# Kernel optimization log

Hardware: AMD Instinct MI355X
Metric: run time of the kernel (lower is better)

The kernel has to match this reference:

```python
import jax, jax.numpy as jnp
import numpy as np

B, N, D, H = 4, 2048, 512, 8
HD = D // H
NUM_BUCKETS, MAX_EXACT, MAX_DIST = 44, 28, 2048
_BAND_RANGES = [range(38, 44), range(34, 40), range(28, 35), range(20, 28),
                range(13, 21), range(7, 14), range(3, 9), range(0, 6)]


def _band_mask():
    m = np.zeros((NUM_BUCKETS, H), dtype=np.float32)
    for h, band in enumerate(_BAND_RANGES):
        for j in band:
            m[j, h] = 1.0
    return jnp.asarray(m)


def _rel_bucket(n):
    # T5-style causal relative-position buckets: exact for d<MAX_EXACT, log-spaced above.
    i = jnp.arange(n)[:, None]
    j = jnp.arange(n)[None, :]
    d = jnp.maximum(i - j, 0)
    safe = jnp.maximum(d, 1).astype(jnp.float32)
    logb = MAX_EXACT + (jnp.log(safe / MAX_EXACT)
                        / np.log(MAX_DIST / MAX_EXACT)
                        * (NUM_BUCKETS - MAX_EXACT)).astype(jnp.int32)
    return jnp.where(d < MAX_EXACT, d, jnp.minimum(logb, NUM_BUCKETS - 1))  # [n,n]


def setup_inputs() -> dict:
    key = jax.random.key(0)
    ks = jax.random.split(key, 12)
    s = 0.02
    return {
        "x": jax.random.normal(ks[0], (B, N, D), jnp.float32),
        "k_delta": jax.random.normal(ks[1], (B, H, N, HD), jnp.float32) * 0.1,
        "v_delta": jax.random.normal(ks[2], (B, H, N, HD), jnp.float32) * 0.1,
        "qkv_w": jax.random.normal(ks[3], (D, 3 * D), jnp.float32) * s,
        "qkv_b": jnp.zeros((3 * D,), jnp.float32),
        "gate_w": jax.random.normal(ks[4], (D, D), jnp.float32) * s,
        "gate_b": jnp.zeros((D,), jnp.float32),
        "out_w": jax.random.normal(ks[5], (D, D), jnp.float32) * s,
        "out_b": jnp.zeros((D,), jnp.float32),
        "pos_bias": jax.random.normal(ks[6], (NUM_BUCKETS, H), jnp.float32) * 0.1,
        "if_gain": jnp.ones((H,), jnp.float32),
    }


def reference(x, k_delta, v_delta, qkv_w, qkv_b, gate_w, gate_b,
              out_w, out_b, pos_bias, if_gain):
    b, n, d = x.shape
    band = _band_mask()
    # hard per-head banding of the relative bias
    eff_bias = pos_bias * band + (1.0 - band) * (-100.0)           # [44,H]
    qkv = x @ qkv_w + qkv_b                                         # [B,N,3D]
    q, k, v = jnp.split(qkv, 3, axis=-1)
    q = q.reshape(b, n, H, HD).transpose(0, 2, 1, 3)                # [B,H,N,HD]
    k = k.reshape(b, n, H, HD).transpose(0, 2, 1, 3) + k_delta
    v = v.reshape(b, n, H, HD).transpose(0, 2, 1, 3) + v_delta
    bucket = _rel_bucket(n)                                         # [N,N] int
    bias = eff_bias[bucket].transpose(2, 0, 1)                      # [H,N,N]
    scores = jnp.einsum("bhid,bhjd->bhij", q, k) / np.sqrt(HD) + bias[None]
    causal = jnp.tril(jnp.ones((n, n), bool))
    scores = jnp.where(causal[None, None], scores, -1e9)
    attn = jax.nn.softmax(scores, axis=-1)
    out = jnp.einsum("bhij,bhjd->bhid", attn, v)                    # [B,H,N,HD]
    out = out * if_gain[None, :, None, None]                        # IF gain
    out_flat = out.transpose(0, 2, 1, 3).reshape(b, n, d)
    gate = jax.nn.sigmoid(x @ gate_w + gate_b)                      # output gating
    return (out_flat * gate) @ out_w + out_b
```

## Files before the change

kernel.cpp:

```cpp
#include <hip/hip_runtime.h>
#include <cmath>

typedef unsigned short u16;
typedef unsigned short u16x4 __attribute__((ext_vector_type(4)));
typedef unsigned short u16x8 __attribute__((ext_vector_type(8)));
typedef __bf16 bf16x8 __attribute__((ext_vector_type(8)));
typedef float f32x4 __attribute__((ext_vector_type(4)));

#define HNUM 8
#define HDIM 64
#define BATCH 4
#define NSEQ 2048
#define DMODEL 512
#define NFUSED 2048
#define LP 72
#define CP 132
#define NSLOT 14

__device__ __forceinline__ u16 f2bf(float f) {
  unsigned int u = __builtin_bit_cast(unsigned int, f);
  u += 0x7fffu + ((u >> 16) & 1u);
  return (u16)(u >> 16);
}

__device__ __forceinline__ float bf2f(u16 v) {
  unsigned int u = ((unsigned int)v) << 16;
  return __builtin_bit_cast(float, u);
}

__device__ __forceinline__ f32x4 mfma_bf16(u16x8 a, u16x8 b, f32x4 c) {
  return __builtin_amdgcn_mfma_f32_16x16x32_bf16(
      __builtin_bit_cast(bf16x8, a), __builtin_bit_cast(bf16x8, b), c, 0, 0, 0);
}

__device__ __forceinline__ void gload16(u16* lds, const u16* g) {
  __builtin_amdgcn_global_load_lds(
      (const __attribute__((address_space(1))) void*)g,
      (__attribute__((address_space(3))) void*)lds, 16, 0, 0);
}

template <int ROWS>
__device__ __forceinline__ void stage_tile(u16* lds, const u16* g, int tid) {
  #pragma unroll
  for (int i = 0; i < ROWS / 64; ++i) {
    const int t = i * 256 + tid;
    const int row = t >> 2;
    const int ch = (t & 3) ^ ((row >> 1) & 3);
    gload16(lds + t * 8, g + (size_t)row * DMODEL + ch * 8);
  }
}
__device__ __forceinline__ int swz_off(int row, int lg) {
  return row * 32 + ((lg ^ ((row >> 1) & 3)) << 3);
}

__global__ __launch_bounds__(256) void cvt_bf16_kernel(
    const float* __restrict__ in, u16* __restrict__ out, int n8) {
  int i = blockIdx.x * 256 + threadIdx.x;
  if (i >= n8) return;
  const float4 f0 = *(const float4*)(in + i * 8);
  const float4 f1 = *(const float4*)(in + i * 8 + 4);
  u16x8 pk;
  pk[0] = f2bf(f0.x); pk[1] = f2bf(f0.y); pk[2] = f2bf(f0.z); pk[3] = f2bf(f0.w);
  pk[4] = f2bf(f1.x); pk[5] = f2bf(f1.y); pk[6] = f2bf(f1.z); pk[7] = f2bf(f1.w);
  *(u16x8*)(out + i * 8) = pk;
}

__global__ __launch_bounds__(256) void transpose_w_kernel(
    const float* __restrict__ W, u16* __restrict__ Wt, int K, int N) {
  __shared__ float tile[32][33];
  const int n0 = blockIdx.x * 32, k0 = blockIdx.y * 32;
  const int tx = threadIdx.x & 31, ty = threadIdx.x >> 5;
  #pragma unroll
  for (int yy = ty; yy < 32; yy += 8)
    tile[yy][tx] = W[(size_t)(k0 + yy) * N + n0 + tx];
  __syncthreads();
  #pragma unroll
  for (int yy = ty; yy < 32; yy += 8)
    Wt[(size_t)(n0 + yy) * K + k0 + tx] = f2bf(tile[tx][yy]);
}

__global__ __launch_bounds__(256) void transpose_v_kernel(
    const u16* __restrict__ v, u16* __restrict__ vT) {
  __shared__ u16 t[64][LP];
  const int n0 = blockIdx.x * 64;
  const size_t bh = blockIdx.y;
  const int r = threadIdx.x >> 2, c0 = (threadIdx.x & 3) << 4;
  const u16* src = v + (bh * NSEQ + n0 + r) * HDIM + c0;
  u16x8 a0 = *(const u16x8*)src;
  u16x8 a1 = *(const u16x8*)(src + 8);
  #pragma unroll
  for (int j = 0; j < 8; ++j) {
    t[c0 + j][r] = a0[j];
    t[c0 + 8 + j][r] = a1[j];
  }
  __syncthreads();
  u16x8 o0 = *(const u16x8*)&t[r][c0];
  u16x8 o1 = *(const u16x8*)&t[r][c0 + 8];
  u16* dst = vT + (bh * HDIM + r) * NSEQ + n0 + c0;
  *(u16x8*)dst = o0;
  *(u16x8*)(dst + 8) = o1;
}

__global__ __launch_bounds__(256) void bias_tab_kernel(
    const float* __restrict__ pos_bias, float* __restrict__ tab) {
  int d = blockIdx.x * 256 + threadIdx.x;
  if (d >= NSEQ) return;
  int bkt;
  if (d < 28) {
    bkt = d;
  } else {
    double t = log((double)d / 28.0) / log(2048.0 / 28.0) * 16.0;
    int ti = 28 + (int)t;
    bkt = ti < 43 ? ti : 43;
  }
  const int lo[8] = {38, 34, 28, 20, 13, 7, 3, 0};
  const int hi[8] = {44, 40, 35, 28, 21, 14, 9, 6};
  #pragma unroll
  for (int h = 0; h < HNUM; ++h) {
    bool inb = (bkt >= lo[h]) && (bkt < hi[h]);
    tab[h * NSEQ + d] = inb ? pos_bias[bkt * HNUM + h] : -100.0f;
  }
}

__global__ __launch_bounds__(256) void gemm_fused(
    const u16* __restrict__ Abf, const u16* __restrict__ Wt,
    const float* __restrict__ qkv_b, const float* __restrict__ gate_b,
    const float* __restrict__ kdelta, const float* __restrict__ vdelta,
    u16* __restrict__ qbf, u16* __restrict__ kbf, u16* __restrict__ vbf,
    u16* __restrict__ gate) {
  __shared__ __align__(16) u16 S[6][128 * 32];

  const int bid = blockIdx.y * 16 + blockIdx.x;
  const int nb = (bid & 7) * 128 + (bid >> 3);
  const int m0 = (nb >> 4) * 128;
  const int n0 = (nb & 15) * 128;

  const int tid = threadIdx.x;
  const int w = tid >> 6, l = tid & 63, li = l & 15, lg = l >> 4;
  const int wr = w >> 1, wc = w & 1;

  f32x4 acc[4][4];
  #pragma unroll
  for (int i = 0; i < 4; ++i)
    #pragma unroll
    for (int j = 0; j < 4; ++j) acc[i][j] = f32x4{0.f, 0.f, 0.f, 0.f};

  const u16* Ab = Abf + (size_t)m0 * DMODEL;
  const u16* Bb = Wt + (size_t)n0 * DMODEL;

  stage_tile<128>(S[0], Ab, tid);
  stage_tile<128>(S[3], Bb, tid);
  stage_tile<128>(S[1], Ab + 32, tid);
  stage_tile<128>(S[4], Bb + 32, tid);

  #pragma unroll
  for (int kt = 0; kt < 16; ++kt) {
    if (kt + 2 < 16) {
      stage_tile<128>(S[(kt + 2) % 3], Ab + (kt + 2) * 32, tid);
      stage_tile<128>(S[3 + (kt + 2) % 3], Bb + (kt + 2) * 32, tid);
    }
    if (kt < 14)       asm volatile("s_waitcnt vmcnt(8)" ::: "memory");
    else if (kt == 14) asm volatile("s_waitcnt vmcnt(4)" ::: "memory");
    else               asm volatile("s_waitcnt vmcnt(0)" ::: "memory");
    __builtin_amdgcn_s_barrier();
    __builtin_amdgcn_sched_barrier(0);
    const u16* Asb = S[kt % 3];
    const u16* Bsb = S[3 + kt % 3];
    u16x8 af[4], bfr[4];
    #pragma unroll
    for (int mt = 0; mt < 4; ++mt)
      af[mt] = *(const u16x8*)&Asb[swz_off(wr * 64 + mt * 16 + li, lg)];
    #pragma unroll
    for (int nt = 0; nt < 4; ++nt)
      bfr[nt] = *(const u16x8*)&Bsb[swz_off(wc * 64 + nt * 16 + li, lg)];
    asm volatile("s_waitcnt lgkmcnt(0)" ::: "memory");
    __builtin_amdgcn_sched_barrier(0);
    #pragma unroll
    for (int mt = 0; mt < 4; ++mt)
      #pragma unroll
      for (int nt = 0; nt < 4; ++nt)
        acc[mt][nt] = mfma_bf16(af[mt], bfr[nt], acc[mt][nt]);
    __builtin_amdgcn_s_barrier();
    __builtin_amdgcn_sched_barrier(0);
  }

  u16* Ct = S[0];
  const int seg = n0 >> 9;
  #pragma unroll
  for (int nt = 0; nt < 4; ++nt) {
    const int col = wc * 64 + nt * 16 + li;
    const int colg = n0 + col;
    const float bv = (seg < 3) ? qkv_b[colg] : gate_b[colg & 511];
    #pragma unroll
    for (int mt = 0; mt < 4; ++mt) {
      const int row = wr * 64 + mt * 16 + lg * 4;
      #pragma unroll
      for (int r = 0; r < 4; ++r)
        Ct[(row + r) * CP + col] = f2bf(acc[mt][nt][r] + bv);
    }
  }
  __syncthreads();

  const int nin = n0 & 511;
  #pragma unroll
  for (int p = 0; p < 8; ++p) {
    const int row = p * 16 + (tid >> 4);
    const int cc = (tid & 15) * 8;
    const int rg = m0 + row;
    const int b = rg >> 11, n = rg & 2047;
    u16x8 cv = *(const u16x8*)&Ct[row * CP + cc];
    if (seg == 3) {
      u16x8 o;
      #pragma unroll
      for (int j = 0; j < 8; ++j)
        o[j] = f2bf(1.f / (1.f + __expf(-bf2f(cv[j]))));
      *(u16x8*)&gate[(size_t)rg * DMODEL + nin + cc] = o;
    } else {
      const int hh = (nin + cc) >> 6, hd = (nin + cc) & 63;
      const size_t hidx = (((size_t)b * HNUM + hh) * NSEQ + n) * HDIM + hd;
      if (seg == 0) {
        u16x8 o;
        #pragma unroll
        for (int j = 0; j < 8; ++j) o[j] = f2bf(bf2f(cv[j]) * 0.125f);
        *(u16x8*)&qbf[hidx] = o;
      } else {
        const float* dp = (seg == 1 ? kdelta : vdelta) + hidx;
        float4 d0 = *(const float4*)dp;
        float4 d1 = *(const float4*)(dp + 4);
        u16x8 o;
        o[0] = f2bf(bf2f(cv[0]) + d0.x); o[1] = f2bf(bf2f(cv[1]) + d0.y);
        o[2] = f2bf(bf2f(cv[2]) + d0.z); o[3] = f2bf(bf2f(cv[3]) + d0.w);
        o[4] = f2bf(bf2f(cv[4]) + d1.x); o[5] = f2bf(bf2f(cv[5]) + d1.y);
        o[6] = f2bf(bf2f(cv[6]) + d1.z); o[7] = f2bf(bf2f(cv[7]) + d1.w);
        *(u16x8*)&((seg == 1) ? kbf : vbf)[hidx] = o;
      }
    }
  }
}

__global__ __launch_bounds__(256) void gemm_out(
    const u16* __restrict__ Abf, const u16* __restrict__ Wt,
    const float* __restrict__ bias, float* __restrict__ outf) {
  __shared__ __align__(16) u16 As[3][64 * 32];
  __shared__ __align__(16) u16 Bs[3][128 * 32];

  const int m0 = blockIdx.y * 64, n0 = blockIdx.x * 128;
  const int tid = threadIdx.x;
  const int w = tid >> 6, l = tid & 63, li = l & 15, lg = l >> 4;
  const int wr = w >> 1, wc = w & 1;

  f32x4 acc[2][4];
  #pragma unroll
  for (int i = 0; i < 2; ++i)
    #pragma unroll
    for (int j = 0; j < 4; ++j) acc[i][j] = f32x4{0.f, 0.f, 0.f, 0.f};

  const u16* Ab = Abf + (size_t)m0 * DMODEL;
  const u16* Bb = Wt + (size_t)n0 * DMODEL;

  stage_tile<64>(As[0], Ab, tid);
  stage_tile<128>(Bs[0], Bb, tid);
  stage_tile<64>(As[1], Ab + 32, tid);
  stage_tile<128>(Bs[1], Bb + 32, tid);

  #pragma unroll
  for (int kt = 0; kt < 16; ++kt) {
    if (kt + 2 < 16) {
      stage_tile<64>(As[(kt + 2) % 3], Ab + (kt + 2) * 32, tid);
      stage_tile<128>(Bs[(kt + 2) % 3], Bb + (kt + 2) * 32, tid);
    }
    if (kt < 14)       asm volatile("s_waitcnt vmcnt(6)" ::: "memory");
    else if (kt == 14) asm volatile("s_waitcnt vmcnt(3)" ::: "memory");
    else               asm volatile("s_waitcnt vmcnt(0)" ::: "memory");
    __builtin_amdgcn_s_barrier();
    __builtin_amdgcn_sched_barrier(0);
    const u16* Asb = As[kt % 3];
    const u16* Bsb = Bs[kt % 3];
    u16x8 af[2], bfr[4];
    #pragma unroll
    for (int mt = 0; mt < 2; ++mt)
      af[mt] = *(const u16x8*)&Asb[swz_off(wr * 32 + mt * 16 + li, lg)];
    #pragma unroll
    for (int nt = 0; nt < 4; ++nt)
      bfr[nt] = *(const u16x8*)&Bsb[swz_off(wc * 64 + nt * 16 + li, lg)];
    asm volatile("s_waitcnt lgkmcnt(0)" ::: "memory");
    __builtin_amdgcn_sched_barrier(0);
    #pragma unroll
    for (int mt = 0; mt < 2; ++mt)
      #pragma unroll
      for (int nt = 0; nt < 4; ++nt)
        acc[mt][nt] = mfma_bf16(af[mt], bfr[nt], acc[mt][nt]);
    __builtin_amdgcn_s_barrier();
    __builtin_amdgcn_sched_barrier(0);
  }

  #pragma unroll
  for (int nt = 0; nt < 4; ++nt) {
    const int colg = n0 + wc * 64 + nt * 16 + li;
    const float bv = bias[colg];
    #pragma unroll
    for (int mt = 0; mt < 2; ++mt) {
      #pragma unroll
      for (int r = 0; r < 4; ++r) {
        const int rowg = m0 + wr * 32 + mt * 16 + lg * 4 + r;
        outf[(size_t)rowg * DMODEL + colg] = acc[mt][nt][r] + bv;
      }
    }
  }
}

__global__ __launch_bounds__(256) void attn_kernel(
    const u16* __restrict__ qbf, const u16* __restrict__ kbf,
    const u16* __restrict__ vbfT, const float* __restrict__ bias_tab,
    const float* __restrict__ if_gain, const u16* __restrict__ gate,
    u16* __restrict__ attn_out, u16* __restrict__ partO,
    float* __restrict__ partM, float* __restrict__ partL) {
  __shared__ __align__(16) u16 Ks[64][LP];
  __shared__ __align__(16) u16 Vt[64][LP];
  __shared__ __align__(16) u16 Pl[4][16][LP];

  static const int DMINW[8] = {408, 139, 26, 18, 11, 5, 1, 0};
  static const int DMAXW[8] = {2049, 702, 185, 29, 22, 15, 10, 7};
  static const int DMINS[8] = {412, 143, 30, 22, 15, 9, 5, 2};
  static const int SH[19] = {0,0,0,0,0,0,0,0, 1,1,1,1, 2,2, 3,4,5,6,7};
  static const int SC[19] = {0,1,2,3,4,5,6,7, 0,1,2,3, 0,1, 0,0,0,0,0};
  static const int SN[19] = {8,8,8,8,8,8,8,8, 4,4,4,4, 2,2, 1,1,1,1,1};

  const int slot = blockIdx.x >> 7;
  const int rem = blockIdx.x & 127;
  const int qt = 31 - (rem >> 2);
  const int b = rem & 3;
  const int h = SH[slot], ch = SC[slot], nc = SN[slot];
  const int bh = b * HNUM + h;
  const int q0 = qt * 64;
  const int tid = threadIdx.x;
  const int w = tid >> 6, l = tid & 63, li = l & 15, lg = l >> 4;

  const u16* qrow = qbf + ((size_t)bh * NSEQ + q0 + w * 16 + li) * HDIM;
  u16x8 qf0 = *(const u16x8*)(qrow + lg * 8);
  u16x8 qf1 = *(const u16x8*)(qrow + 32 + lg * 8);

  const bool pure = q0 >= DMINS[h];
  int kv_lo = 0, kv_hi = q0 + 64;
  if (pure) {
    int lo = q0 - DMAXW[h];
    kv_lo = (lo > 0 ? lo : 0) & ~63;
    kv_hi = q0 + 64 - DMINW[h];
  }
  const int t0 = kv_lo >> 6, t1 = (kv_hi - 1) >> 6;
  const int len = t1 - t0 + 1;
  const int ta = t0 + (len * ch) / nc;
  const int tb = t0 + (len * (ch + 1)) / nc - 1;

  const int srow = tid >> 2;
  const int scb = (tid & 3) << 4;
  const float* btab = bias_tab + h * NSEQ;

  float mrun = -INFINITY, lrun = 0.f;
  f32x4 O[4] = {{0.f,0.f,0.f,0.f},{0.f,0.f,0.f,0.f},
                {0.f,0.f,0.f,0.f},{0.f,0.f,0.f,0.f}};

  for (int tt = ta; tt <= tb; ++tt) {
    const int kv0 = tt << 6;
    {
      const size_t kbase = ((size_t)bh * NSEQ + kv0 + srow) * HDIM + scb;
      u16x8 k0 = *(const u16x8*)(kbf + kbase);
      u16x8 k1 = *(const u16x8*)(kbf + kbase + 8);
      const size_t vbase = ((size_t)bh * HDIM + srow) * NSEQ + kv0 + scb;
      u16x8 v0 = *(const u16x8*)(vbfT + vbase);
      u16x8 v1 = *(const u16x8*)(vbfT + vbase + 8);
      *(u16x8*)&Ks[srow][scb] = k0;
      *(u16x8*)&Ks[srow][scb + 8] = k1;
      *(u16x8*)&Vt[srow][scb] = v0;
      *(u16x8*)&Vt[srow][scb + 8] = v1;
    }
    __syncthreads();

    f32x4 s[4];
    #pragma unroll
    for (int t = 0; t < 4; ++t) {
      u16x8 a0 = *(const u16x8*)&Ks[t * 16 + li][lg * 8];
      u16x8 a1 = *(const u16x8*)&Ks[t * 16 + li][32 + lg * 8];
      f32x4 acc = {0.f, 0.f, 0.f, 0.f};
      acc = mfma_bf16(a0, qf0, acc);
      acc = mfma_bf16(a1, qf1, acc);
      s[t] = acc;
    }

    const int D0 = (q0 + w * 16 + li) - kv0 - lg * 4;
    float rm = -1e30f;
    #pragma unroll
    for (int t = 0; t < 4; ++t) {
      #pragma unroll
      for (int r = 0; r < 4; ++r) {
        int d = D0 - 16 * t - r;
        float sv = s[t][r];
        sv = (d >= 0) ? (sv + btab[d]) : -1e30f;
        s[t][r] = sv;
        rm = fmaxf(rm, sv);
      }
    }
    rm = fmaxf(rm, __shfl_xor(rm, 16, 64));
    rm = fmaxf(rm, __shfl_xor(rm, 32, 64));
    const float mn = fmaxf(mrun, rm);
    const float f = __expf(mrun - mn);
    mrun = mn;
    float ps = 0.f;
    #pragma unroll
    for (int t = 0; t < 4; ++t) {
      #pragma unroll
      for (int r = 0; r < 4; ++r) {
        float p = __expf(s[t][r] - mn);
        s[t][r] = p;
        ps += p;
      }
    }
    ps += __shfl_xor(ps, 16, 64);
    ps += __shfl_xor(ps, 32, 64);
    lrun = lrun * f + ps;

    #pragma unroll
    for (int t = 0; t < 4; ++t) {
      u16x4 pk;
      pk[0] = f2bf(s[t][0]); pk[1] = f2bf(s[t][1]);
      pk[2] = f2bf(s[t][2]); pk[3] = f2bf(s[t][3]);
      *(u16x4*)&Pl[w][li][t * 16 + lg * 4] = pk;
    }

    float fr[4];
    #pragma unroll
    for (int r = 0; r < 4; ++r) fr[r] = __shfl(f, lg * 4 + r, 64);
    #pragma unroll
    for (int dt = 0; dt < 4; ++dt) {
      O[dt][0] *= fr[0]; O[dt][1] *= fr[1];
      O[dt][2] *= fr[2]; O[dt][3] *= fr[3];
    }
    __syncthreads();

    #pragma unroll
    for (int ks = 0; ks < 2; ++ks) {
      u16x8 pA = *(const u16x8*)&Pl[w][li][ks * 32 + lg * 8];
      #pragma unroll
      for (int dt = 0; dt < 4; ++dt) {
        u16x8 vB = *(const u16x8*)&Vt[dt * 16 + li][ks * 32 + lg * 8];
        O[dt] = mfma_bf16(pA, vB, O[dt]);
      }
    }
    __syncthreads();
  }

  if (nc == 1) {
    const float gain = if_gain[h];
    float linv[4];
    #pragma unroll
    for (int r = 0; r < 4; ++r)
      linv[r] = gain / __shfl(lrun, lg * 4 + r, 64);
    #pragma unroll
    for (int r = 0; r < 4; ++r) {
      const int i = q0 + w * 16 + lg * 4 + r;
      const size_t base = ((size_t)b * NSEQ + i) * DMODEL + h * HDIM + li;
      #pragma unroll
      for (int dt = 0; dt < 4; ++dt) {
        const float g = bf2f(gate[base + dt * 16]);
        attn_out[base + dt * 16] = f2bf(O[dt][r] * linv[r] * g);
      }
    }
  } else {
    const int sbase = (b * 32 + qt) * NSLOT + slot;
    #pragma unroll
    for (int r = 0; r < 4; ++r) {
      const int rl = w * 16 + lg * 4 + r;
      #pragma unroll
      for (int dt = 0; dt < 4; ++dt)
        partO[(size_t)sbase * 4096 + rl * 64 + dt * 16 + li] = f2bf(O[dt][r]);
    }
    if (lg == 0) {
      partM[sbase * 64 + w * 16 + li] = mrun;
      partL[sbase * 64 + w * 16 + li] = lrun;
    }
  }
}

__global__ __launch_bounds__(256) void combine_kernel(
    const u16* __restrict__ partO, const float* __restrict__ partM,
    const float* __restrict__ partL, const float* __restrict__ if_gain,
    const u16* __restrict__ gate, u16* __restrict__ attn_out) {
  const int b = blockIdx.x & 3, qt = blockIdx.x >> 2;
  const int tid = threadIdx.x;
  const int row = tid >> 2, d0 = (tid & 3) << 4;
  static const int HNC[3] = {8, 4, 2};
  static const int HS0[3] = {0, 8, 12};

  #pragma unroll
  for (int hc = 0; hc < 3; ++hc) {
    const int nc = HNC[hc], s0 = HS0[hc];
    const int sbase = (b * 32 + qt) * NSLOT + s0;
    float m[8];
    float M = -INFINITY;
    #pragma unroll
    for (int c = 0; c < 8; ++c) {
      m[c] = (c < nc) ? partM[(sbase + c) * 64 + row] : -INFINITY;
      M = fmaxf(M, m[c]);
    }
    float wch[8];
    float den = 0.f;
    #pragma unroll
    for (int c = 0; c < 8; ++c) {
      wch[c] = (c < nc) ? __expf(m[c] - M) : 0.f;
      if (c < nc) den += wch[c] * partL[(sbase + c) * 64 + row];
    }
    float num[16];
    #pragma unroll
    for (int j = 0; j < 16; ++j) num[j] = 0.f;
    #pragma unroll
    for (int c = 0; c < 8; ++c) {
      if (c < nc) {
        const u16* op = partO + (size_t)(sbase + c) * 4096 + row * 64 + d0;
        u16x8 o0 = *(const u16x8*)op;
        u16x8 o1 = *(const u16x8*)(op + 8);
        #pragma unroll
        for (int j = 0; j < 8; ++j) {
          num[j]     += wch[c] * bf2f(o0[j]);
          num[8 + j] += wch[c] * bf2f(o1[j]);
        }
      }
    }
    const float inv = if_gain[hc] / den;
    const size_t obase =
        ((size_t)b * NSEQ + qt * 64 + row) * DMODEL + hc * HDIM + d0;
    u16x8 g0 = *(const u16x8*)(gate + obase);
    u16x8 g1 = *(const u16x8*)(gate + obase + 8);
    u16x8 r0, r1;
    #pragma unroll
    for (int j = 0; j < 8; ++j) {
      r0[j] = f2bf(num[j] * inv * bf2f(g0[j]));
      r1[j] = f2bf(num[8 + j] * inv * bf2f(g1[j]));
    }
    *(u16x8*)(attn_out + obase) = r0;
    *(u16x8*)(attn_out + obase + 8) = r1;
  }
}

extern "C" void kernel_launch(void* const* d_in, const int* in_sizes, int n_in,
                              void* d_out, int out_size, void* d_ws,
                              size_t ws_size, hipStream_t stream) {
  const float* x       = (const float*)d_in[0];
  const float* k_delta = (const float*)d_in[1];
  const float* v_delta = (const float*)d_in[2];
  const float* qkv_w   = (const float*)d_in[3];
  const float* qkv_b   = (const float*)d_in[4];
  const float* gate_w  = (const float*)d_in[5];
  const float* gate_b  = (const float*)d_in[6];
  const float* out_w   = (const float*)d_in[7];
  const float* out_b   = (const float*)d_in[8];
  const float* pos_bias = (const float*)d_in[9];
  const float* if_gain  = (const float*)d_in[10];
  float* out = (float*)d_out;
  char* ws = (char*)d_ws;

  u16*   xbf      = (u16*)(ws + 0);
  u16*   qbf      = (u16*)(ws + 8388608);
  u16*   kbf      = (u16*)(ws + 16777216);
  u16*   vbf      = (u16*)(ws + 25165824);
  u16*   vbfT     = (u16*)(ws + 33554432);
  u16*   gate_buf = (u16*)(ws + 41943040);
  u16*   fused_wt = (u16*)(ws + 50331648);
  u16*   out_wt   = (u16*)(ws + 52428800);
  float* bias_tab = (float*)(ws + 52953088);
  u16*   partO = (u16*)(ws + 53018624);
  float* partM = (float*)(ws + 67698688);
  float* partL = (float*)(ws + 68157440);
  u16*   attn_buf = vbf;

  cvt_bf16_kernel<<<dim3(2048), dim3(256), 0, stream>>>(
      x, xbf, BATCH * NSEQ * DMODEL / 8);
  transpose_w_kernel<<<dim3(48, 16), dim3(256), 0, stream>>>(
      qkv_w, fused_wt, DMODEL, 3 * DMODEL);
  transpose_w_kernel<<<dim3(16, 16), dim3(256), 0, stream>>>(
      gate_w, fused_wt + (size_t)3 * DMODEL * DMODEL, DMODEL, DMODEL);
  transpose_w_kernel<<<dim3(16, 16), dim3(256), 0, stream>>>(
      out_w, out_wt, DMODEL, DMODEL);
  bias_tab_kernel<<<dim3(8), dim3(256), 0, stream>>>(pos_bias, bias_tab);

  gemm_fused<<<dim3(16, 64), dim3(256), 0, stream>>>(
      xbf, fused_wt, qkv_b, gate_b, k_delta, v_delta,
      qbf, kbf, vbf, gate_buf);

  transpose_v_kernel<<<dim3(32, 32), dim3(256), 0, stream>>>(vbf, vbfT);

  attn_kernel<<<dim3(2432), dim3(256), 0, stream>>>(
      qbf, kbf, vbfT, bias_tab, if_gain, gate_buf, attn_buf,
      partO, partM, partL);

  combine_kernel<<<dim3(128), dim3(256), 0, stream>>>(
      partO, partM, partL, if_gain, gate_buf, attn_buf);

  gemm_out<<<dim3(4, 128), dim3(256), 0, stream>>>(
      attn_buf, out_wt, out_b, out);

  (void)in_sizes; (void)n_in; (void)out_size; (void)ws_size;
}
```

Measured before the change: 100.9 us.

## Enlarge fused QKV/gate GEMM tiles to 256x256 with 512 threads and BK=64

The fused projection GEMM moves from 128x128 tiles with 256 threads and a triple-buffered BK=32 pipeline to 256x256 tiles with 512 threads, double-buffered BK=64 stages and an 8-way XOR swizzle. The epilogue is written out in two 128-row halves through a padded LDS staging buffer. The larger tile raises arithmetic intensity and halves global reloads of A and B. In exchange it uses 128KB of LDS and 128 accumulator registers per thread, which limits occupancy, and it launches only 256 blocks, close to the CU count.

```diff
diff --git a/kernel.cpp b/kernel.cpp
--- a/kernel.cpp
+++ b/kernel.cpp
@@ -14,7 +14,7 @@
 #define DMODEL 512
 #define NFUSED 2048
 #define LP 72
-#define CP 132
+#define CPE 272
 #define NSLOT 14
 
 __device__ __forceinline__ u16 f2bf(float f) {
@@ -37,6 +37,18 @@
   __builtin_amdgcn_global_load_lds(
       (const __attribute__((address_space(1))) void*)g,
       (__attribute__((address_space(3))) void*)lds, 16, 0, 0);
+}
+
+__device__ __forceinline__ void stage256(u16* lds, const u16* g, int tid) {
+  #pragma unroll
+  for (int i = 0; i < 4; ++i) {
+    const int s = i * 512 + tid;
+    const int row = s >> 3, ch = s & 7;
+    gload16(lds + s * 8, g + (size_t)row * DMODEL + ((ch ^ (row & 7)) << 3));
+  }
+}
+__device__ __forceinline__ int swz64(int row, int c) {
+  return row * 64 + ((c ^ (row & 7)) << 3);
 }
 
 template <int ROWS>
@@ -122,119 +134,127 @@
   }
 }
 
-__global__ __launch_bounds__(256) void gemm_fused(
+__global__ __launch_bounds__(512) void gemm_fused(
     const u16* __restrict__ Abf, const u16* __restrict__ Wt,
     const float* __restrict__ qkv_b, const float* __restrict__ gate_b,
     const float* __restrict__ kdelta, const float* __restrict__ vdelta,
     u16* __restrict__ qbf, u16* __restrict__ kbf, u16* __restrict__ vbf,
     u16* __restrict__ gate) {
-  __shared__ __align__(16) u16 S[6][128 * 32];
-
-  const int bid = blockIdx.y * 16 + blockIdx.x;
-  const int nb = (bid & 7) * 128 + (bid >> 3);
-  const int m0 = (nb >> 4) * 128;
-  const int n0 = (nb & 15) * 128;
+  __shared__ __align__(16) u16 S[65536];
+  u16* SA[2] = {S, S + 16384};
+  u16* SB[2] = {S + 32768, S + 49152};
+
+  const int bid = blockIdx.x;
+  const int m0 = ((bid & 7) * 4 + ((bid >> 3) & 3)) * 256;
+  const int n0 = (bid >> 5) * 256;
 
   const int tid = threadIdx.x;
   const int w = tid >> 6, l = tid & 63, li = l & 15, lg = l >> 4;
-  const int wr = w >> 1, wc = w & 1;
-
-  f32x4 acc[4][4];
-  #pragma unroll
-  for (int i = 0; i < 4; ++i)
+  const int wm = w >> 2, wn = w & 3;
+
+  f32x4 acc[8][4];
+  #pragma unroll
+  for (int i = 0; i < 8; ++i)
     #pragma unroll
     for (int j = 0; j < 4; ++j) acc[i][j] = f32x4{0.f, 0.f, 0.f, 0.f};
 
   const u16* Ab = Abf + (size_t)m0 * DMODEL;
   const u16* Bb = Wt + (size_t)n0 * DMODEL;
 
-  stage_tile<128>(S[0], Ab, tid);
-  stage_tile<128>(S[3], Bb, tid);
-  stage_tile<128>(S[1], Ab + 32, tid);
-  stage_tile<128>(S[4], Bb + 32, tid);
-
-  #pragma unroll
-  for (int kt = 0; kt < 16; ++kt) {
-    if (kt + 2 < 16) {
-      stage_tile<128>(S[(kt + 2) % 3], Ab + (kt + 2) * 32, tid);
-      stage_tile<128>(S[3 + (kt + 2) % 3], Bb + (kt + 2) * 32, tid);
-    }
-    if (kt < 14)       asm volatile("s_waitcnt vmcnt(8)" ::: "memory");
-    else if (kt == 14) asm volatile("s_waitcnt vmcnt(4)" ::: "memory");
-    else               asm volatile("s_waitcnt vmcnt(0)" ::: "memory");
+  stage256(SA[0], Ab, tid);
+  stage256(SB[0], Bb, tid);
+
+  #pragma unroll
+  for (int kt = 0; kt < 8; ++kt) {
+    if (kt < 7) {
+      stage256(SA[(kt + 1) & 1], Ab + (kt + 1) * 64, tid);
+      stage256(SB[(kt + 1) & 1], Bb + (kt + 1) * 64, tid);
+      asm volatile("s_waitcnt vmcnt(8)" ::: "memory");
+    } else {
+      asm volatile("s_waitcnt vmcnt(0)" ::: "memory");
+    }
     __builtin_amdgcn_s_barrier();
     __builtin_amdgcn_sched_barrier(0);
-    const u16* Asb = S[kt % 3];
-    const u16* Bsb = S[3 + kt % 3];
-    u16x8 af[4], bfr[4];
-    #pragma unroll
-    for (int mt = 0; mt < 4; ++mt)
-      af[mt] = *(const u16x8*)&Asb[swz_off(wr * 64 + mt * 16 + li, lg)];
-    #pragma unroll
-    for (int nt = 0; nt < 4; ++nt)
-      bfr[nt] = *(const u16x8*)&Bsb[swz_off(wc * 64 + nt * 16 + li, lg)];
-    asm volatile("s_waitcnt lgkmcnt(0)" ::: "memory");
-    __builtin_amdgcn_sched_barrier(0);
-    #pragma unroll
-    for (int mt = 0; mt < 4; ++mt)
+    const u16* Asb = SA[kt & 1];
+    const u16* Bsb = SB[kt & 1];
+    #pragma unroll
+    for (int ks = 0; ks < 2; ++ks) {
+      u16x8 a[8], b[4];
+      #pragma unroll
+      for (int mt = 0; mt < 8; ++mt)
+        a[mt] = *(const u16x8*)&Asb[swz64(wm * 128 + mt * 16 + li, ks * 4 + lg)];
       #pragma unroll
       for (int nt = 0; nt < 4; ++nt)
-        acc[mt][nt] = mfma_bf16(af[mt], bfr[nt], acc[mt][nt]);
+        b[nt] = *(const u16x8*)&Bsb[swz64(wn * 64 + nt * 16 + li, ks * 4 + lg)];
+      asm volatile("s_waitcnt lgkmcnt(0)" ::: "memory");
+      __builtin_amdgcn_sched_barrier(0);
+      #pragma unroll
+      for (int mt = 0; mt < 8; ++mt)
+        #pragma unroll
+        for (int nt = 0; nt < 4; ++nt)
+          acc[mt][nt] = mfma_bf16(a[mt], b[nt], acc[mt][nt]);
+    }
     __builtin_amdgcn_s_barrier();
     __builtin_amdgcn_sched_barrier(0);
   }
 
-  u16* Ct = S[0];
+  u16* Ct = S;
   const int seg = n0 >> 9;
-  #pragma unroll
-  for (int nt = 0; nt < 4; ++nt) {
-    const int col = wc * 64 + nt * 16 + li;
-    const int colg = n0 + col;
-    const float bv = (seg < 3) ? qkv_b[colg] : gate_b[colg & 511];
-    #pragma unroll
-    for (int mt = 0; mt < 4; ++mt) {
-      const int row = wr * 64 + mt * 16 + lg * 4;
-      #pragma unroll
-      for (int r = 0; r < 4; ++r)
-        Ct[(row + r) * CP + col] = f2bf(acc[mt][nt][r] + bv);
-    }
-  }
-  __syncthreads();
-
   const int nin = n0 & 511;
   #pragma unroll
-  for (int p = 0; p < 8; ++p) {
-    const int row = p * 16 + (tid >> 4);
-    const int cc = (tid & 15) * 8;
-    const int rg = m0 + row;
-    const int b = rg >> 11, n = rg & 2047;
-    u16x8 cv = *(const u16x8*)&Ct[row * CP + cc];
-    if (seg == 3) {
-      u16x8 o;
-      #pragma unroll
-      for (int j = 0; j < 8; ++j)
-        o[j] = f2bf(1.f / (1.f + __expf(-bf2f(cv[j]))));
-      *(u16x8*)&gate[(size_t)rg * DMODEL + nin + cc] = o;
-    } else {
-      const int hh = (nin + cc) >> 6, hd = (nin + cc) & 63;
-      const size_t hidx = (((size_t)b * HNUM + hh) * NSEQ + n) * HDIM + hd;
-      if (seg == 0) {
+  for (int h = 0; h < 2; ++h) {
+    if (wm == h) {
+      #pragma unroll
+      for (int nt = 0; nt < 4; ++nt) {
+        const int col = wn * 64 + nt * 16 + li;
+        const int colg = n0 + col;
+        const float bv = (seg < 3) ? qkv_b[colg] : gate_b[colg & 511];
+        #pragma unroll
+        for (int mt = 0; mt < 8; ++mt) {
+          const int row = mt * 16 + lg * 4;
+          #pragma unroll
+          for (int r = 0; r < 4; ++r)
+            Ct[(row + r) * CPE + col] = f2bf(acc[mt][nt][r] + bv);
+        }
+      }
+    }
+    __syncthreads();
+    #pragma unroll
+    for (int p = 0; p < 8; ++p) {
+      const int idx = p * 512 + tid;
+      const int row = idx >> 5, ccol = (idx & 31) * 8;
+      const int rg = m0 + h * 128 + row;
+      const int bb = rg >> 11, n = rg & 2047;
+      u16x8 cv = *(const u16x8*)&Ct[row * CPE + ccol];
+      const int cws = nin + ccol;
+      if (seg == 3) {
         u16x8 o;
         #pragma unroll
-        for (int j = 0; j < 8; ++j) o[j] = f2bf(bf2f(cv[j]) * 0.125f);
-        *(u16x8*)&qbf[hidx] = o;
+        for (int j = 0; j < 8; ++j)
+          o[j] = f2bf(1.f / (1.f + __expf(-bf2f(cv[j]))));
+        *(u16x8*)&gate[(size_t)rg * DMODEL + cws] = o;
       } else {
-        const float* dp = (seg == 1 ? kdelta : vdelta) + hidx;
-        float4 d0 = *(const float4*)dp;
-        float4 d1 = *(const float4*)(dp + 4);
-        u16x8 o;
-        o[0] = f2bf(bf2f(cv[0]) + d0.x); o[1] = f2bf(bf2f(cv[1]) + d0.y);
-        o[2] = f2bf(bf2f(cv[2]) + d0.z); o[3] = f2bf(bf2f(cv[3]) + d0.w);
-        o[4] = f2bf(bf2f(cv[4]) + d1.x); o[5] = f2bf(bf2f(cv[5]) + d1.y);
-        o[6] = f2bf(bf2f(cv[6]) + d1.z); o[7] = f2bf(bf2f(cv[7]) + d1.w);
-        *(u16x8*)&((seg == 1) ? kbf : vbf)[hidx] = o;
-      }
-    }
+        const int hh = cws >> 6, hd = cws & 63;
+        const size_t hidx = (((size_t)bb * HNUM + hh) * NSEQ + n) * HDIM + hd;
+        if (seg == 0) {
+          u16x8 o;
+          #pragma unroll
+          for (int j = 0; j < 8; ++j) o[j] = f2bf(bf2f(cv[j]) * 0.125f);
+          *(u16x8*)&qbf[hidx] = o;
+        } else {
+          const float* dp = (seg == 1 ? kdelta : vdelta) + hidx;
+          float4 d0 = *(const float4*)dp;
+          float4 d1 = *(const float4*)(dp + 4);
+          u16x8 o;
+          o[0] = f2bf(bf2f(cv[0]) + d0.x); o[1] = f2bf(bf2f(cv[1]) + d0.y);
+          o[2] = f2bf(bf2f(cv[2]) + d0.z); o[3] = f2bf(bf2f(cv[3]) + d0.w);
+          o[4] = f2bf(bf2f(cv[4]) + d1.x); o[5] = f2bf(bf2f(cv[5]) + d1.y);
+          o[6] = f2bf(bf2f(cv[6]) + d1.z); o[7] = f2bf(bf2f(cv[7]) + d1.w);
+          *(u16x8*)&((seg == 1) ? kbf : vbf)[hidx] = o;
+        }
+      }
+    }
+    __syncthreads();
   }
 }
 
@@ -582,7 +602,7 @@
       out_w, out_wt, DMODEL, DMODEL);
   bias_tab_kernel<<<dim3(8), dim3(256), 0, stream>>>(pos_bias, bias_tab);
 
-  gemm_fused<<<dim3(16, 64), dim3(256), 0, stream>>>(
+  gemm_fused<<<dim3(256), dim3(512), 0, stream>>>(
       xbf, fused_wt, qkv_b, gate_b, k_delta, v_delta,
       qbf, kbf, vbf, gate_buf);
 
```

After: 98.54 us. 1.02x faster.

## Widen fused QKV/gate GEMM tile to 128x256 with 512 threads; merge weight transposes

Applied to the files above, without the earlier changes.

The fused projection GEMM moves from 128x128 tiles with 4 waves to 128x256 tiles with 8 waves in 512-thread blocks. This halves the grid and raises reuse of each staged A tile, and it uses a new XCD-aware block mapping and a staging helper. The three weight-transpose launches are merged into one kernel to cut launch overhead. The larger LDS footprint and 512-thread blocks may reduce occupancy.

```diff
diff --git a/kernel.cpp b/kernel.cpp
--- a/kernel.cpp
+++ b/kernel.cpp
@@ -12,9 +12,8 @@
 #define BATCH 4
 #define NSEQ 2048
 #define DMODEL 512
-#define NFUSED 2048
 #define LP 72
-#define CP 132
+#define CPE 264
 #define NSLOT 14
 
 __device__ __forceinline__ u16 f2bf(float f) {
@@ -37,6 +36,10 @@
   __builtin_amdgcn_global_load_lds(
       (const __attribute__((address_space(1))) void*)g,
       (__attribute__((address_space(3))) void*)lds, 16, 0, 0);
+}
+
+__device__ __forceinline__ int swz_off(int row, int lg) {
+  return row * 32 + ((lg ^ ((row >> 1) & 3)) << 3);
 }
 
 template <int ROWS>
@@ -49,8 +52,22 @@
     gload16(lds + t * 8, g + (size_t)row * DMODEL + ch * 8);
   }
 }
-__device__ __forceinline__ int swz_off(int row, int lg) {
-  return row * 32 + ((lg ^ ((row >> 1) & 3)) << 3);
+
+__device__ __forceinline__ void stageAB(u16* ldsA, u16* ldsB, const u16* gA,
+                                        const u16* gB, int tid) {
+  {
+    const int s = tid;
+    const int row = s >> 2;
+    const int ch = (s & 3) ^ ((row >> 1) & 3);
+    gload16(ldsA + s * 8, gA + (size_t)row * DMODEL + ch * 8);
+  }
+  #pragma unroll
+  for (int i = 0; i < 2; ++i) {
+    const int s = i * 512 + tid;
+    const int row = s >> 2;
+    const int ch = (s & 3) ^ ((row >> 1) & 3);
+    gload16(ldsB + s * 8, gB + (size_t)row * DMODEL + ch * 8);
+  }
 }
 
 __global__ __launch_bounds__(256) void cvt_bf16_kernel(
@@ -65,10 +82,19 @@
   *(u16x8*)(out + i * 8) = pk;
 }
 
-__global__ __launch_bounds__(256) void transpose_w_kernel(
-    const float* __restrict__ W, u16* __restrict__ Wt, int K, int N) {
+__global__ __launch_bounds__(256) void transpose_wall(
+    const float* __restrict__ qkv_w, const float* __restrict__ gate_w,
+    const float* __restrict__ out_w, u16* __restrict__ fused_wt,
+    u16* __restrict__ out_wt) {
   __shared__ float tile[32][33];
-  const int n0 = blockIdx.x * 32, k0 = blockIdx.y * 32;
+  const int bx = blockIdx.x;
+  const float* W;
+  u16* Wt;
+  int N, nb;
+  if (bx < 48)      { W = qkv_w;  Wt = fused_wt;                     N = 1536; nb = bx; }
+  else if (bx < 64) { W = gate_w; Wt = fused_wt + (size_t)1536 * 512; N = 512;  nb = bx - 48; }
+  else              { W = out_w;  Wt = out_wt;                       N = 512;  nb = bx - 64; }
+  const int n0 = nb * 32, k0 = blockIdx.y * 32;
   const int tx = threadIdx.x & 31, ty = threadIdx.x >> 5;
   #pragma unroll
   for (int yy = ty; yy < 32; yy += 8)
@@ -76,7 +102,7 @@
   __syncthreads();
   #pragma unroll
   for (int yy = ty; yy < 32; yy += 8)
-    Wt[(size_t)(n0 + yy) * K + k0 + tx] = f2bf(tile[tx][yy]);
+    Wt[(size_t)(n0 + yy) * DMODEL + k0 + tx] = f2bf(tile[tx][yy]);
 }
 
 __global__ __launch_bounds__(256) void transpose_v_kernel(
@@ -122,22 +148,24 @@
   }
 }
 
-__global__ __launch_bounds__(256) void gemm_fused(
+__global__ __launch_bounds__(512, 4) void gemm_fused(
     const u16* __restrict__ Abf, const u16* __restrict__ Wt,
     const float* __restrict__ qkv_b, const float* __restrict__ gate_b,
     const float* __restrict__ kdelta, const float* __restrict__ vdelta,
     u16* __restrict__ qbf, u16* __restrict__ kbf, u16* __restrict__ vbf,
     u16* __restrict__ gate) {
-  __shared__ __align__(16) u16 S[6][128 * 32];
-
-  const int bid = blockIdx.y * 16 + blockIdx.x;
-  const int nb = (bid & 7) * 128 + (bid >> 3);
-  const int m0 = (nb >> 4) * 128;
-  const int n0 = (nb & 15) * 128;
+  __shared__ __align__(16) u16 S[36864];
+  u16* SA3[3] = {S, S + 4096, S + 8192};
+  u16* SB3[3] = {S + 12288, S + 20480, S + 28672};
+
+  const int bid = blockIdx.x;
+  const int xcd = bid & 7, loc = bid >> 3;
+  const int m0 = (xcd * 8 + (loc & 7)) * 128;
+  const int n0 = (loc >> 3) * 256;
 
   const int tid = threadIdx.x;
   const int w = tid >> 6, l = tid & 63, li = l & 15, lg = l >> 4;
-  const int wr = w >> 1, wc = w & 1;
+  const int wm = w >> 2, wn = w & 3;
 
   f32x4 acc[4][4];
   #pragma unroll
@@ -148,31 +176,28 @@
   const u16* Ab = Abf + (size_t)m0 * DMODEL;
   const u16* Bb = Wt + (size_t)n0 * DMODEL;
 
-  stage_tile<128>(S[0], Ab, tid);
-  stage_tile<128>(S[3], Bb, tid);
-  stage_tile<128>(S[1], Ab + 32, tid);
-  stage_tile<128>(S[4], Bb + 32, tid);
+  stageAB(SA3[0], SB3[0], Ab, Bb, tid);
+  stageAB(SA3[1], SB3[1], Ab + 32, Bb + 32, tid);
 
   #pragma unroll
   for (int kt = 0; kt < 16; ++kt) {
-    if (kt + 2 < 16) {
-      stage_tile<128>(S[(kt + 2) % 3], Ab + (kt + 2) * 32, tid);
-      stage_tile<128>(S[3 + (kt + 2) % 3], Bb + (kt + 2) * 32, tid);
-    }
-    if (kt < 14)       asm volatile("s_waitcnt vmcnt(8)" ::: "memory");
-    else if (kt == 14) asm volatile("s_waitcnt vmcnt(4)" ::: "memory");
+    if (kt + 2 < 16)
+      stageAB(SA3[(kt + 2) % 3], SB3[(kt + 2) % 3],
+              Ab + (kt + 2) * 32, Bb + (kt + 2) * 32, tid);
+    if (kt < 14)       asm volatile("s_waitcnt vmcnt(6)" ::: "memory");
+    else if (kt == 14) asm volatile("s_waitcnt vmcnt(3)" ::: "memory");
     else               asm volatile("s_waitcnt vmcnt(0)" ::: "memory");
     __builtin_amdgcn_s_barrier();
     __builtin_amdgcn_sched_barrier(0);
-    const u16* Asb = S[kt % 3];
-    const u16* Bsb = S[3 + kt % 3];
+    const u16* Asb = SA3[kt % 3];
+    const u16* Bsb = SB3[kt % 3];
     u16x8 af[4], bfr[4];
     #pragma unroll
     for (int mt = 0; mt < 4; ++mt)
-      af[mt] = *(const u16x8*)&Asb[swz_off(wr * 64 + mt * 16 + li, lg)];
+      af[mt] = *(const u16x8*)&Asb[swz_off(wm * 64 + mt * 16 + li, lg)];
     #pragma unroll
     for (int nt = 0; nt < 4; ++nt)
-      bfr[nt] = *(const u16x8*)&Bsb[swz_off(wc * 64 + nt * 16 + li, lg)];
+      bfr[nt] = *(const u16x8*)&Bsb[swz_off(wn * 64 + nt * 16 + li, lg)];
     asm volatile("s_waitcnt lgkmcnt(0)" ::: "memory");
     __builtin_amdgcn_sched_barrier(0);
     #pragma unroll
@@ -184,40 +209,41 @@
     __builtin_amdgcn_sched_barrier(0);
   }
 
-  u16* Ct = S[0];
+  u16* Ct = S;
   const int seg = n0 >> 9;
+  const int nin = n0 & 511;
   #pragma unroll
   for (int nt = 0; nt < 4; ++nt) {
-    const int col = wc * 64 + nt * 16 + li;
+    const int col = wn * 64 + nt * 16 + li;
     const int colg = n0 + col;
     const float bv = (seg < 3) ? qkv_b[colg] : gate_b[colg & 511];
     #pragma unroll
     for (int mt = 0; mt < 4; ++mt) {
-      const int row = wr * 64 + mt * 16 + lg * 4;
+      const int row = wm * 64 + mt * 16 + lg * 4;
       #pragma unroll
       for (int r = 0; r < 4; ++r)
-        Ct[(row + r) * CP + col] = f2bf(acc[mt][nt][r] + bv);
+        Ct[(row + r) * CPE + col] = f2bf(acc[mt][nt][r] + bv);
     }
   }
   __syncthreads();
 
-  const int nin = n0 & 511;
   #pragma unroll
   for (int p = 0; p < 8; ++p) {
-    const int row = p * 16 + (tid >> 4);
-    const int cc = (tid & 15) * 8;
+    const int idx = p * 512 + tid;
+    const int row = idx >> 5, ccol = (idx & 31) * 8;
     const int rg = m0 + row;
-    const int b = rg >> 11, n = rg & 2047;
-    u16x8 cv = *(const u16x8*)&Ct[row * CP + cc];
+    const int bb = rg >> 11, n = rg & 2047;
+    u16x8 cv = *(const u16x8*)&Ct[row * CPE + ccol];
+    const int cws = nin + ccol;
     if (seg == 3) {
       u16x8 o;
       #pragma unroll
       for (int j = 0; j < 8; ++j)
         o[j] = f2bf(1.f / (1.f + __expf(-bf2f(cv[j]))));
-      *(u16x8*)&gate[(size_t)rg * DMODEL + nin + cc] = o;
+      *(u16x8*)&gate[(size_t)rg * DMODEL + cws] = o;
     } else {
-      const int hh = (nin + cc) >> 6, hd = (nin + cc) & 63;
-      const size_t hidx = (((size_t)b * HNUM + hh) * NSEQ + n) * HDIM + hd;
+      const int hh = cws >> 6, hd = cws & 63;
+      const size_t hidx = (((size_t)bb * HNUM + hh) * NSEQ + n) * HDIM + hd;
       if (seg == 0) {
         u16x8 o;
         #pragma unroll
@@ -574,15 +600,11 @@
 
   cvt_bf16_kernel<<<dim3(2048), dim3(256), 0, stream>>>(
       x, xbf, BATCH * NSEQ * DMODEL / 8);
-  transpose_w_kernel<<<dim3(48, 16), dim3(256), 0, stream>>>(
-      qkv_w, fused_wt, DMODEL, 3 * DMODEL);
-  transpose_w_kernel<<<dim3(16, 16), dim3(256), 0, stream>>>(
-      gate_w, fused_wt + (size_t)3 * DMODEL * DMODEL, DMODEL, DMODEL);
-  transpose_w_kernel<<<dim3(16, 16), dim3(256), 0, stream>>>(
-      out_w, out_wt, DMODEL, DMODEL);
+  transpose_wall<<<dim3(80, 16), dim3(256), 0, stream>>>(
+      qkv_w, gate_w, out_w, fused_wt, out_wt);
   bias_tab_kernel<<<dim3(8), dim3(256), 0, stream>>>(pos_bias, bias_tab);
 
-  gemm_fused<<<dim3(16, 64), dim3(256), 0, stream>>>(
+  gemm_fused<<<dim3(512), dim3(512), 0, stream>>>(
       xbf, fused_wt, qkv_b, gate_b, k_delta, v_delta,
       qbf, kbf, vbf, gate_buf);
 
```

Result: faster. 91.81 us (-9.0%).
